# Kernel tuning notes

Measured on AMD Instinct MI355X. Metric: run time of the kernel, lower is better.

The kernel has to match this reference:

```python
import jax, jax.numpy as jnp
import numpy as np

B, T, S, I, H = 512, 256, 64, 32, 1024


def _kaiming(key, shape):
    fan_in = shape[1]
    return jax.random.normal(key, shape, dtype=jnp.float32) * jnp.sqrt(2.0 / fan_in)


def setup_inputs() -> dict:
    key = jax.random.key(0)
    k_x0, k_u, k1, k2, k3 = jax.random.split(key, 5)
    return {
        "x0": jax.random.normal(k_x0, (B, 1, S), dtype=jnp.float32),
        "u": jax.random.normal(k_u, (B, T, I), dtype=jnp.float32),
        "W1": _kaiming(k1, (H, S + I)),
        "b1": jnp.zeros((H,), dtype=jnp.float32),
        "W2": _kaiming(k2, (H, H)),
        "b2": jnp.zeros((H,), dtype=jnp.float32),
        "W3": _kaiming(k3, (S, H)),
        "b3": jnp.zeros((S,), dtype=jnp.float32),
    }


def reference(x0, u, W1, b1, W2, b2, W3, b3):
    # x0: (B,1,S) -> state (B,S); u: (B,T,I)
    def step(x, u_t):  # x: (B,S), u_t: (B,I)
        h = jax.nn.sigmoid(jnp.concatenate([x, u_t], axis=-1) @ W1.T + b1)
        h = jax.nn.sigmoid(h @ W2.T + b2)
        x_new = h @ W3.T + b3  # (B,S)
        return x_new, x_new

    _, ys = jax.lax.scan(step, x0[:, 0, :], jnp.swapaxes(u, 0, 1))  # ys: (T,B,S)
    return jnp.swapaxes(ys, 0, 1)  # (B,T,S)
```

## Files before the change

### kernel.cpp

```cpp
#include <hip/hip_runtime.h>
#include <hip/hip_bf16.h>

#define BB 512
#define TT 256
#define SS 64
#define II 32
#define HH 1024
#define K1 96
#define KS1 3
#define KS2 32

#define W1P_ELEMS (64 * KS1 * 512)
#define W2P_ELEMS (64 * KS2 * 512)
#define W3P_ELEMS (4  * KS2 * 512)
#define PACK_TOTAL (W1P_ELEMS + W2P_ELEMS + W3P_ELEMS)

#define MBG 32
#define NBG 8
#define SLOTBUF (MBG * NBG * 16 * 64)

#define OFF_W1P   0
#define OFF_W2P   (OFF_W1P + W1P_ELEMS*2)
#define OFF_W3P   (OFF_W2P + W2P_ELEMS*2)
#define OFF_SLOT  (OFF_W3P + W3P_ELEMS*2)
#define OFF_FL    (OFF_SLOT + 2*SLOTBUF*4)

typedef _Float16 f16x8 __attribute__((ext_vector_type(8)));
typedef _Float16 f16x4 __attribute__((ext_vector_type(4)));
typedef float f32x4 __attribute__((ext_vector_type(4)));
typedef unsigned long long u64;

__global__ void pack_weights(const float* __restrict__ W1,
                             const float* __restrict__ W2,
                             const float* __restrict__ W3,
                             _Float16* __restrict__ W1p,
                             _Float16* __restrict__ W2p,
                             _Float16* __restrict__ W3p)
{
    int idx = blockIdx.x * 256 + threadIdx.x;
    if (idx >= PACK_TOTAL) return;
    const float* src;
    _Float16* dst;
    int K, e;
    if (idx < W1P_ELEMS)                 { src = W1; dst = W1p; K = K1; e = idx; }
    else if (idx < W1P_ELEMS + W2P_ELEMS){ src = W2; dst = W2p; K = HH; e = idx - W1P_ELEMS; }
    else                                 { src = W3; dst = W3p; K = HH; e = idx - W1P_ELEMS - W2P_ELEMS; }
    int j    = e & 7;
    int lane = (e >> 3) & 63;
    int f    = e >> 9;
    int KSw  = K / 32;
    int nt   = f / KSw;
    int ks   = f - nt * KSw;
    int n    = nt * 16 + (lane & 15);
    int k    = ks * 32 + ((lane >> 4) << 3) + j;
    dst[e] = (_Float16)src[(size_t)n * K + k];
}

__device__ __forceinline__ void st_h16(unsigned char* base, int pitch, int row, int col, _Float16 v) {
    int off = (row * pitch + col * 2) ^ ((row & 7) << 4);
    *(_Float16*)(base + off) = v;
}
__device__ __forceinline__ void st_b64l(unsigned char* base, int pitch, int row, int col, u64 v) {
    int off = (row * pitch + col * 2) ^ ((row & 7) << 4);
    *(u64*)(base + off) = v;
}
__device__ __forceinline__ uint4 ld_b128(const unsigned char* base, int pitch, int row, int col) {
    int off = (row * pitch + col * 2) ^ ((row & 7) << 4);
    return *(const uint4*)(base + off);
}
__device__ __forceinline__ f16x8 ld_frag_lds(const unsigned char* base, int pitch, int row, int k0) {
    return __builtin_bit_cast(f16x8, ld_b128(base, pitch, row, k0));
}
__device__ __forceinline__ f16x8 ldg_frag(const _Float16* __restrict__ p, int fragIdx, int lane) {
    const uint4* q = (const uint4*)(p + (size_t)fragIdx * 512) + lane;
    return __builtin_bit_cast(f16x8, *q);
}
__device__ __forceinline__ float sigmoidf_fast(float z) {
    return 1.0f / (1.0f + __expf(-z));
}
__device__ __forceinline__ u64 pack4h(float a, float b, float c, float d) {
    f16x4 p; p[0]=(_Float16)a; p[1]=(_Float16)b; p[2]=(_Float16)c; p[3]=(_Float16)d;
    return __builtin_bit_cast(u64, p);
}

#define PIN_AGPR(x) asm("" : "+a"(x))
#define MFMA_AV(acc, aFrag, bAgpr) \
    asm("v_mfma_f32_16x16x32_f16 %0, %1, %2, %0" : "+v"(acc) : "v"(aFrag), "a"(bAgpr))

__device__ __forceinline__ u64 ldg_u64(const u64* p) {
    return __hip_atomic_load((u64*)p, __ATOMIC_RELAXED, __HIP_MEMORY_SCOPE_AGENT);
}
__device__ __forceinline__ void stg_f32(float* p, float v) {
    __hip_atomic_store(p, v, __ATOMIC_RELAXED, __HIP_MEMORY_SCOPE_AGENT);
}
__device__ __forceinline__ int ldg_flag(int* p) {
    return __hip_atomic_load(p, __ATOMIC_RELAXED, __HIP_MEMORY_SCOPE_AGENT);
}
__device__ __forceinline__ void stg_flag(int* p, int v) {
    __hip_atomic_store(p, v, __ATOMIC_RELAXED, __HIP_MEMORY_SCOPE_AGENT);
}
__device__ __forceinline__ void spin_ge(int* f, int target, volatile int* dead) {
    if (*dead) return;
    int it = 0;
    while (ldg_flag(f) < target) {
        __builtin_amdgcn_s_sleep(1);
        if (++it > 400000) { *dead = 1; break; }
    }
}

__global__ __launch_bounds__(256, 1) void rnn_main(
    const float* __restrict__ x0, const float* __restrict__ u,
    const float* __restrict__ b1, const float* __restrict__ b2, const float* __restrict__ b3,
    const _Float16* __restrict__ W1p, const _Float16* __restrict__ W2p, const _Float16* __restrict__ W3p,
    float* __restrict__ slots, int* __restrict__ slotflag,
    float* __restrict__ out)
{
    __shared__ __align__(16) unsigned char sH1A[16 * 2048];
    __shared__ __align__(16) unsigned char sXC [16 * 256];
    __shared__ __align__(16) unsigned char sH2 [16 * 256];
    __shared__ int sDead;

    const int tid  = threadIdx.x;
    const int lane = tid & 63;
    const int w    = tid >> 6;
    const int bid  = blockIdx.x;
    const int mb   = bid & 31;
    const int nb   = bid >> 5;
    const int b0   = mb * 16;
    const int col  = lane & 15;
    const int g    = lane >> 4;

    const int ntA = nb * 8 + w * 2;
    const int ntB = ntA + 1;
    f16x8 w2f[64];
    #pragma unroll
    for (int ks = 0; ks < KS2; ++ks) {
        w2f[ks] = ldg_frag(W2p, ntA * KS2 + ks, lane);
        PIN_AGPR(w2f[ks]);
    }
    #pragma unroll
    for (int ks = 0; ks < KS2; ++ks) {
        w2f[32 + ks] = ldg_frag(W2p, ntB * KS2 + ks, lane);
        PIN_AGPR(w2f[32 + ks]);
    }

    float b1v[16];
    #pragma unroll
    for (int j = 0; j < 16; ++j) b1v[j] = b1[(w * 16 + j) * 16 + col];
    const float b2va = b2[ntA * 16 + col];
    const float b2vb = b2[ntB * 16 + col];

    const int gm = tid >> 4;
    const int gs = (tid & 15) * 4;
    float b3v[4];
    #pragma unroll
    for (int i = 0; i < 4; ++i) b3v[i] = b3[gs + i];

    int* myFL = slotflag + mb * 8;

    if (tid == 0) sDead = 0;
    __syncthreads();

    for (int t = 0;; ++t) {
        if (t < TT && tid >= 128) {
            int tr = tid - 128;
            int m = tr >> 3, i4 = tr & 7;
            const float* up = u + ((size_t)(b0 + m) * TT + t) * II + i4 * 4;
            float4 uv = *(const float4*)up;
            st_b64l(sXC, 256, m, 64 + i4 * 4, pack4h(uv.x, uv.y, uv.z, uv.w));
        }
        if (t > 0 && tid < 8) spin_ge(&myFL[tid], t, &sDead);
        __syncthreads();

        if (t == 0) {
            const float* xp = x0 + (size_t)(b0 + gm) * SS + gs;
            float4 pa = *(const float4*)xp;
            st_b64l(sXC, 256, gm, gs, pack4h(pa.x, pa.y, pa.z, pa.w));
        } else {
            const float* sb = slots + (size_t)((t - 1) & 1) * SLOTBUF;
            float s0 = b3v[0], s1 = b3v[1], s2 = b3v[2], s3 = b3v[3];
            #pragma unroll
            for (int nb2 = 0; nb2 < 8; ++nb2) {
                const u64* sp = (const u64*)(sb + ((size_t)(mb * 8 + nb2) * 16 + gm) * 64 + gs);
                float2 fa = __builtin_bit_cast(float2, ldg_u64(sp));
                float2 fb = __builtin_bit_cast(float2, ldg_u64(sp + 1));
                s0 += fa.x; s1 += fa.y; s2 += fb.x; s3 += fb.y;
            }
            if (nb == 0) {
                float* op = out + ((size_t)(b0 + gm) * TT + (t - 1)) * SS + gs;
                *(float4*)op = make_float4(s0, s1, s2, s3);
            }
            if (t < TT)
                st_b64l(sXC, 256, gm, gs, pack4h(s0, s1, s2, s3));
        }
        if (t == TT) break;
        __syncthreads();

        {
            f16x8 af[KS1];
            #pragma unroll
            for (int ks = 0; ks < KS1; ++ks)
                af[ks] = ld_frag_lds(sXC, 256, col, ks * 32 + g * 8);
            #pragma unroll
            for (int p = 0; p < 2; ++p) {
                f32x4 acc[8];
                #pragma unroll
                for (int i = 0; i < 8; ++i) acc[i] = (f32x4){0.f, 0.f, 0.f, 0.f};
                f16x8 wf[8][KS1];
                #pragma unroll
                for (int i = 0; i < 8; ++i)
                    #pragma unroll
                    for (int ks = 0; ks < KS1; ++ks)
                        wf[i][ks] = ldg_frag(W1p, (w * 16 + p * 8 + i) * KS1 + ks, lane);
                #pragma unroll
                for (int ks = 0; ks < KS1; ++ks)
                    #pragma unroll
                    for (int i = 0; i < 8; ++i)
                        asm("v_mfma_f32_16x16x32_f16 %0, %1, %2, %0"
                            : "+v"(acc[i]) : "v"(af[ks]), "v"(wf[i][ks]));
                asm volatile("s_nop 7\n\ts_nop 7"
                             : "+v"(acc[0]), "+v"(acc[1]), "+v"(acc[2]), "+v"(acc[3]),
                               "+v"(acc[4]), "+v"(acc[5]), "+v"(acc[6]), "+v"(acc[7]));
                #pragma unroll
                for (int i = 0; i < 8; ++i) {
                    int n = (w * 16 + p * 8 + i) * 16 + col;
                    #pragma unroll
                    for (int r = 0; r < 4; ++r)
                        st_h16(sH1A, 2048, g * 4 + r, n,
                               (_Float16)sigmoidf_fast(acc[i][r] + b1v[p * 8 + i]));
                }
            }
        }
        f16x8 w3f[4];
        #pragma unroll
        for (int ksl = 0; ksl < 4; ++ksl)
            w3f[ksl] = ldg_frag(W3p, w * KS2 + nb * 4 + ksl, lane);
        __syncthreads();

        {
            f32x4 aA0 = (f32x4){0.f,0.f,0.f,0.f}, aA1 = (f32x4){0.f,0.f,0.f,0.f};
            f32x4 aB0 = (f32x4){0.f,0.f,0.f,0.f}, aB1 = (f32x4){0.f,0.f,0.f,0.f};
            #pragma unroll
            for (int ks = 0; ks < KS2; ks += 2) {
                f16x8 a0 = ld_frag_lds(sH1A, 2048, col, ks * 32 + g * 8);
                f16x8 a1 = ld_frag_lds(sH1A, 2048, col, (ks + 1) * 32 + g * 8);
                MFMA_AV(aA0, a0, w2f[ks]);
                MFMA_AV(aB0, a0, w2f[32 + ks]);
                MFMA_AV(aA1, a1, w2f[ks + 1]);
                MFMA_AV(aB1, a1, w2f[32 + ks + 1]);
            }
            asm volatile("s_nop 7\n\ts_nop 7"
                         : "+v"(aA0), "+v"(aA1), "+v"(aB0), "+v"(aB1));
            #pragma unroll
            for (int r = 0; r < 4; ++r) {
                st_h16(sH2, 256, g * 4 + r, (w * 2) * 16 + col,
                       (_Float16)sigmoidf_fast(aA0[r] + aA1[r] + b2va));
                st_h16(sH2, 256, g * 4 + r, (w * 2 + 1) * 16 + col,
                       (_Float16)sigmoidf_fast(aB0[r] + aB1[r] + b2vb));
            }
        }
        __syncthreads();

        {
            f32x4 a3 = (f32x4){0.f, 0.f, 0.f, 0.f};
            #pragma unroll
            for (int ksl = 0; ksl < 4; ++ksl) {
                f16x8 a = ld_frag_lds(sH2, 256, col, ksl * 32 + g * 8);
                asm("v_mfma_f32_16x16x32_f16 %0, %1, %2, %0"
                    : "+v"(a3) : "v"(a), "v"(w3f[ksl]));
            }
            asm volatile("s_nop 7\n\ts_nop 7" : "+v"(a3));
            float* sbw = slots + (size_t)(t & 1) * SLOTBUF;
            #pragma unroll
            for (int r = 0; r < 4; ++r)
                stg_f32(&sbw[((size_t)(mb * 8 + nb) * 16 + g * 4 + r) * 64 + w * 16 + col], a3[r]);
        }
        __syncthreads();
        if (tid == 0) stg_flag(&myFL[nb], t + 1);
    }
}

extern "C" void kernel_launch(void* const* d_in, const int* in_sizes, int n_in,
                              void* d_out, int out_size, void* d_ws, size_t ws_size,
                              hipStream_t stream) {
    const float* x0 = (const float*)d_in[0];
    const float* u  = (const float*)d_in[1];
    const float* W1 = (const float*)d_in[2];
    const float* b1 = (const float*)d_in[3];
    const float* W2 = (const float*)d_in[4];
    const float* b2 = (const float*)d_in[5];
    const float* W3 = (const float*)d_in[6];
    const float* b3 = (const float*)d_in[7];
    float* out = (float*)d_out;

    char* ws = (char*)d_ws;
    _Float16* W1p  = (_Float16*)(ws + OFF_W1P);
    _Float16* W2p  = (_Float16*)(ws + OFF_W2P);
    _Float16* W3p  = (_Float16*)(ws + OFF_W3P);
    float*    slots= (float*)   (ws + OFF_SLOT);
    int*      slfl = (int*)     (ws + OFF_FL);

    hipMemsetAsync(ws + OFF_FL, 0, 1024, stream);
    pack_weights<<<(PACK_TOTAL + 255) / 256, 256, 0, stream>>>(W1, W2, W3, W1p, W2p, W3p);
    rnn_main<<<MBG * NBG, 256, 0, stream>>>(x0, u, b1, b2, b3, W1p, W2p, W3p,
                                            slots, slfl, out);
}
```

Measured before the change: 2.666 ms.

## Hoist input-projection MFMAs and W1 loads ahead of the cross-block spin wait

The W1 contribution from the external input u_t is now computed per step before the block waits on the inter-block flags. The u fragment is loaded directly into registers instead of going through shared memory. The first half of the W1 state-weight fragments is also prefetched before the wait, and the second half is loaded while the first half's MFMAs run. This moves independent work off the serial recurrence critical path and shrinks the shared state buffer. In exchange it needs 16 live accumulators plus prefetched fragments, which raises VGPR pressure next to the 64 AGPR-pinned W2 fragments.

```diff
diff --git a/kernel.cpp b/kernel.cpp
--- a/kernel.cpp
+++ b/kernel.cpp
@@ -86,6 +86,8 @@
 #define PIN_AGPR(x) asm("" : "+a"(x))
 #define MFMA_AV(acc, aFrag, bAgpr) \
     asm("v_mfma_f32_16x16x32_f16 %0, %1, %2, %0" : "+v"(acc) : "v"(aFrag), "a"(bAgpr))
+#define MFMA_VV(acc, aFrag, bVgpr) \
+    asm("v_mfma_f32_16x16x32_f16 %0, %1, %2, %0" : "+v"(acc) : "v"(aFrag), "v"(bVgpr))
 
 __device__ __forceinline__ u64 ldg_u64(const u64* p) {
     return __hip_atomic_load((u64*)p, __ATOMIC_RELAXED, __HIP_MEMORY_SCOPE_AGENT);
@@ -116,7 +118,7 @@
     float* __restrict__ out)
 {
     __shared__ __align__(16) unsigned char sH1A[16 * 2048];
-    __shared__ __align__(16) unsigned char sXC [16 * 256];
+    __shared__ __align__(16) unsigned char sXC [16 * 128];
     __shared__ __align__(16) unsigned char sH2 [16 * 256];
     __shared__ int sDead;
 
@@ -156,26 +158,46 @@
     #pragma unroll
     for (int i = 0; i < 4; ++i) b3v[i] = b3[gs + i];
 
+    const float* uBase = u + ((size_t)(b0 + col) * TT) * II + g * 8;
+
     int* myFL = slotflag + mb * 8;
 
     if (tid == 0) sDead = 0;
     __syncthreads();
 
     for (int t = 0;; ++t) {
-        if (t < TT && tid >= 128) {
-            int tr = tid - 128;
-            int m = tr >> 3, i4 = tr & 7;
-            const float* up = u + ((size_t)(b0 + m) * TT + t) * II + i4 * 4;
-            float4 uv = *(const float4*)up;
-            st_b64l(sXC, 256, m, 64 + i4 * 4, pack4h(uv.x, uv.y, uv.z, uv.w));
-        }
+        f32x4 acc[16];
+        if (t < TT) {
+            const float* up = uBase + (size_t)t * II;
+            float4 ua = *(const float4*)up;
+            float4 ub = *(const float4*)(up + 4);
+            f16x8 au;
+            au[0]=(_Float16)ua.x; au[1]=(_Float16)ua.y; au[2]=(_Float16)ua.z; au[3]=(_Float16)ua.w;
+            au[4]=(_Float16)ub.x; au[5]=(_Float16)ub.y; au[6]=(_Float16)ub.z; au[7]=(_Float16)ub.w;
+            #pragma unroll
+            for (int i = 0; i < 16; ++i) acc[i] = (f32x4){0.f, 0.f, 0.f, 0.f};
+            #pragma unroll
+            for (int i = 0; i < 16; ++i) {
+                f16x8 wu = ldg_frag(W1p, (w * 16 + i) * KS1 + 2, lane);
+                MFMA_VV(acc[i], au, wu);
+            }
+        }
+        f16x8 w1xA[8][2];
+        if (t < TT) {
+            #pragma unroll
+            for (int i = 0; i < 8; ++i) {
+                w1xA[i][0] = ldg_frag(W1p, (w * 16 + i) * KS1 + 0, lane);
+                w1xA[i][1] = ldg_frag(W1p, (w * 16 + i) * KS1 + 1, lane);
+            }
+        }
+
         if (t > 0 && tid < 8) spin_ge(&myFL[tid], t, &sDead);
         __syncthreads();
 
         if (t == 0) {
             const float* xp = x0 + (size_t)(b0 + gm) * SS + gs;
             float4 pa = *(const float4*)xp;
-            st_b64l(sXC, 256, gm, gs, pack4h(pa.x, pa.y, pa.z, pa.w));
+            st_b64l(sXC, 128, gm, gs, pack4h(pa.x, pa.y, pa.z, pa.w));
         } else {
             const float* sb = slots + (size_t)((t - 1) & 1) * SLOTBUF;
             float s0 = b3v[0], s1 = b3v[1], s2 = b3v[2], s3 = b3v[3];
@@ -191,44 +213,51 @@
                 *(float4*)op = make_float4(s0, s1, s2, s3);
             }
             if (t < TT)
-                st_b64l(sXC, 256, gm, gs, pack4h(s0, s1, s2, s3));
+                st_b64l(sXC, 128, gm, gs, pack4h(s0, s1, s2, s3));
         }
         if (t == TT) break;
         __syncthreads();
 
         {
-            f16x8 af[KS1];
-            #pragma unroll
-            for (int ks = 0; ks < KS1; ++ks)
-                af[ks] = ld_frag_lds(sXC, 256, col, ks * 32 + g * 8);
-            #pragma unroll
-            for (int p = 0; p < 2; ++p) {
-                f32x4 acc[8];
+            f16x8 af0 = ld_frag_lds(sXC, 128, col, 0 * 32 + g * 8);
+            f16x8 af1 = ld_frag_lds(sXC, 128, col, 1 * 32 + g * 8);
+            f16x8 w1xB[8][2];
+            #pragma unroll
+            for (int i = 0; i < 8; ++i) {
+                w1xB[i][0] = ldg_frag(W1p, (w * 16 + 8 + i) * KS1 + 0, lane);
+                w1xB[i][1] = ldg_frag(W1p, (w * 16 + 8 + i) * KS1 + 1, lane);
+            }
+            #pragma unroll
+            for (int i = 0; i < 8; ++i) {
+                MFMA_VV(acc[i], af0, w1xA[i][0]);
+                MFMA_VV(acc[i], af1, w1xA[i][1]);
+            }
+            asm volatile("s_nop 7\n\ts_nop 7"
+                         : "+v"(acc[0]), "+v"(acc[1]), "+v"(acc[2]), "+v"(acc[3]),
+                           "+v"(acc[4]), "+v"(acc[5]), "+v"(acc[6]), "+v"(acc[7]));
+            #pragma unroll
+            for (int i = 0; i < 8; ++i) {
+                int n = (w * 16 + i) * 16 + col;
                 #pragma unroll
-                for (int i = 0; i < 8; ++i) acc[i] = (f32x4){0.f, 0.f, 0.f, 0.f};
-                f16x8 wf[8][KS1];
+                for (int r = 0; r < 4; ++r)
+                    st_h16(sH1A, 2048, g * 4 + r, n,
+                           (_Float16)sigmoidf_fast(acc[i][r] + b1v[i]));
+            }
+            #pragma unroll
+            for (int i = 0; i < 8; ++i) {
+                MFMA_VV(acc[8 + i], af0, w1xB[i][0]);
+                MFMA_VV(acc[8 + i], af1, w1xB[i][1]);
+            }
+            asm volatile("s_nop 7\n\ts_nop 7"
+                         : "+v"(acc[8]), "+v"(acc[9]), "+v"(acc[10]), "+v"(acc[11]),
+                           "+v"(acc[12]), "+v"(acc[13]), "+v"(acc[14]), "+v"(acc[15]));
+            #pragma unroll
+            for (int i = 0; i < 8; ++i) {
+                int n = (w * 16 + 8 + i) * 16 + col;
                 #pragma unroll
-                for (int i = 0; i < 8; ++i)
-                    #pragma unroll
-                    for (int ks = 0; ks < KS1; ++ks)
-                        wf[i][ks] = ldg_frag(W1p, (w * 16 + p * 8 + i) * KS1 + ks, lane);
-                #pragma unroll
-                for (int ks = 0; ks < KS1; ++ks)
-                    #pragma unroll
-                    for (int i = 0; i < 8; ++i)
-                        asm("v_mfma_f32_16x16x32_f16 %0, %1, %2, %0"
-                            : "+v"(acc[i]) : "v"(af[ks]), "v"(wf[i][ks]));
-                asm volatile("s_nop 7\n\ts_nop 7"
-                             : "+v"(acc[0]), "+v"(acc[1]), "+v"(acc[2]), "+v"(acc[3]),
-                               "+v"(acc[4]), "+v"(acc[5]), "+v"(acc[6]), "+v"(acc[7]));
-                #pragma unroll
-                for (int i = 0; i < 8; ++i) {
-                    int n = (w * 16 + p * 8 + i) * 16 + col;
-                    #pragma unroll
-                    for (int r = 0; r < 4; ++r)
-                        st_h16(sH1A, 2048, g * 4 + r, n,
-                               (_Float16)sigmoidf_fast(acc[i][r] + b1v[p * 8 + i]));
-                }
+                for (int r = 0; r < 4; ++r)
+                    st_h16(sH1A, 2048, g * 4 + r, n,
+                           (_Float16)sigmoidf_fast(acc[8 + i][r] + b1v[8 + i]));
             }
         }
         f16x8 w3f[4];
@@ -266,8 +295,7 @@
             #pragma unroll
             for (int ksl = 0; ksl < 4; ++ksl) {
                 f16x8 a = ld_frag_lds(sH2, 256, col, ksl * 32 + g * 8);
-                asm("v_mfma_f32_16x16x32_f16 %0, %1, %2, %0"
-                    : "+v"(a3) : "v"(a), "v"(w3f[ksl]));
+                MFMA_VV(a3, a, w3f[ksl]);
             }
             asm volatile("s_nop 7\n\ts_nop 7" : "+v"(a3));
             float* sbw = slots + (size_t)(t & 1) * SLOTBUF;
```

New measurement: 6.432 ms. +141.2%, slower.
